# Performance work log

Measured on AMD Instinct MI355X. Metric: run time of the kernel, lower is better.

The kernel has to match this reference:

```python
import jax, jax.numpy as jnp
import numpy as np

B, C, H, W = 16, 128, 32, 32
CHOICES, OUT_C, OH, OW = 4, 128, 32, 32
INIT_WEIGHTS = [0.25, 0.25, 0.25, 0.25]
INIT_STD = 0.01


def setup_inputs() -> dict:
    key = jax.random.key(0)
    ks = jax.random.split(key, 6)
    x = jax.random.normal(ks[0], (B, C, H, W), dtype=jnp.float32)
    # 1x1 conv1d weights == dense matrices [out, in]; xavier-normal-ish scale
    Wq = jax.random.normal(ks[1], (C, C), dtype=jnp.float32) * (1.0 / np.sqrt(C))
    Wk = jax.random.normal(ks[2], (C, C), dtype=jnp.float32) * (1.0 / np.sqrt(C))
    Wv = jax.random.normal(ks[3], (CHOICES * OUT_C, C), dtype=jnp.float32) * (1.0 / np.sqrt(C))
    gamma = jnp.ones((1,), dtype=jnp.float32)  # learnable scalar (0 at init; use 1 to exercise math)
    # mask init: per-choice mean = init_weights[i] * out_choices, std = init_std
    means = jnp.asarray([w * CHOICES for w in INIT_WEIGHTS], dtype=jnp.float32)
    mask = jax.random.normal(ks[4], (1, OUT_C, OH, OW, CHOICES), dtype=jnp.float32) * INIT_STD + means
    return {"x": x, "Wq": Wq, "Wk": Wk, "Wv": Wv, "gamma": gamma, "mask": mask}


def reference(x, Wq, Wk, Wv, gamma, mask):
    b, c, h, w = x.shape
    n = h * w
    x2 = x.reshape(b, c, n)                                   # [b, C, N]
    f = jnp.einsum('oc,bcn->bon', Wq, x2)                     # query  [b, C, N]
    g = jnp.einsum('oc,bcn->bon', Wk, x2)                     # key    [b, C, N]
    hv = jnp.einsum('oc,bcn->bon', Wv, x2)                    # value  [b, CHOICES*OUT_C, N]
    # beta = softmax(f^T g) over dim 1 (rows), per torch code
    scores = jnp.einsum('bcn,bcm->bnm', f, g)                 # [b, N, N]
    beta = jax.nn.softmax(scores, axis=1)
    out = gamma * jnp.einsum('bkn,bnm->bkm', hv, beta)        # [b, CHOICES*OUT_C, N]
    out = out.reshape(b, CHOICES, OUT_C, OH, OW)              # no resize: H==OH, W==OW
    out = jnp.transpose(out, (0, 2, 3, 4, 1))                 # [b, OUT_C, OH, OW, CHOICES]
    return out + mask
```

## Files before the change

### kernel.cpp

```cpp
#include <hip/hip_runtime.h>

#define B 16
#define C 128
#define NN 1024
#define KV 512
#define CHO 4

typedef _Float16 f16x8 __attribute__((ext_vector_type(8)));
typedef float f32x4 __attribute__((ext_vector_type(4)));

__device__ __forceinline__ unsigned short f2h(float v) {
  _Float16 h = (_Float16)v;
  return __builtin_bit_cast(unsigned short, h);
}
__device__ __forceinline__ unsigned int packh2(float a, float b) {
  return (unsigned int)f2h(a) | ((unsigned int)f2h(b) << 16);
}

__global__ __launch_bounds__(256) void proj_kernel(
    const float* __restrict__ x, const float* __restrict__ Wq,
    const float* __restrict__ Wk, const float* __restrict__ Wv,
    unsigned short* __restrict__ fT, unsigned short* __restrict__ gT,
    unsigned short* __restrict__ hv)
{
  const int nt = blockIdx.x, rt = blockIdx.y, b = blockIdx.z;
  const int r0 = rt * 64, n0 = nt * 64;
  __shared__ __align__(16) float Wt[64][132];
  __shared__ __align__(16) float Xt[128][68];
  const int t = threadIdx.x;

  const float* Wbase; int roff;
  if (r0 < 128)      { Wbase = Wq; roff = r0; }
  else if (r0 < 256) { Wbase = Wk; roff = r0 - 128; }
  else               { Wbase = Wv; roff = r0 - 256; }

  #pragma unroll
  for (int i = 0; i < 8; ++i) {
    int idx = t + i * 256;
    int row = idx >> 5, c4 = (idx & 31) * 4;
    float4 v = *reinterpret_cast<const float4*>(Wbase + (size_t)(roff + row) * C + c4);
    *reinterpret_cast<float4*>(&Wt[row][c4]) = v;
  }
  #pragma unroll
  for (int i = 0; i < 8; ++i) {
    int idx = t + i * 256;
    int row = idx >> 4, c4 = (idx & 15) * 4;
    float4 v = *reinterpret_cast<const float4*>(x + (size_t)(b * C + row) * NN + n0 + c4);
    *reinterpret_cast<float4*>(&Xt[row][c4]) = v;
  }
  __syncthreads();

  const int tr = t >> 4, tc = t & 15;
  float acc[4][4];
  #pragma unroll
  for (int i = 0; i < 4; ++i)
    #pragma unroll
    for (int j = 0; j < 4; ++j) acc[i][j] = 0.f;

  for (int k = 0; k < C; k += 4) {
    float4 wv[4], xv[4];
    #pragma unroll
    for (int i = 0; i < 4; ++i) wv[i] = *reinterpret_cast<const float4*>(&Wt[tr * 4 + i][k]);
    #pragma unroll
    for (int kk = 0; kk < 4; ++kk) xv[kk] = *reinterpret_cast<const float4*>(&Xt[k + kk][tc * 4]);
    #pragma unroll
    for (int i = 0; i < 4; ++i) {
      float wi[4] = { wv[i].x, wv[i].y, wv[i].z, wv[i].w };
      #pragma unroll
      for (int kk = 0; kk < 4; ++kk) {
        float xk[4] = { xv[kk].x, xv[kk].y, xv[kk].z, xv[kk].w };
        acc[i][0] += wi[kk] * xk[0];
        acc[i][1] += wi[kk] * xk[1];
        acc[i][2] += wi[kk] * xk[2];
        acc[i][3] += wi[kk] * xk[3];
      }
    }
  }

  if (r0 < 256) {
    unsigned short* dst = (r0 < 128) ? fT : gT;
    #pragma unroll
    for (int j = 0; j < 4; ++j) {
      ushort4 o = { f2h(acc[0][j]), f2h(acc[1][j]), f2h(acc[2][j]), f2h(acc[3][j]) };
      *reinterpret_cast<ushort4*>(dst + ((size_t)(b * NN) + n0 + tc * 4 + j) * C + roff + tr * 4) = o;
    }
  } else {
    #pragma unroll
    for (int i = 0; i < 4; ++i) {
      ushort4 o = { f2h(acc[i][0]), f2h(acc[i][1]), f2h(acc[i][2]), f2h(acc[i][3]) };
      *reinterpret_cast<ushort4*>(hv + ((size_t)(b * KV) + roff + tr * 4 + i) * NN + n0 + tc * 4) = o;
    }
  }
}

__global__ __launch_bounds__(256, 2) void attn_kernel(
    const unsigned short* __restrict__ fT, const unsigned short* __restrict__ gT,
    const unsigned short* __restrict__ hv, const float* __restrict__ gamma,
    const float* __restrict__ mask, float* __restrict__ out)
{
  const int t  = threadIdx.x;
  const int w  = t >> 6;
  const int l  = t & 63;
  const int lg = l >> 4;
  const int lm = l & 15;
  const int b  = blockIdx.y;
  const int m0 = blockIdx.x * 64;

  __shared__ unsigned short P_lds[64][40];
  __shared__ float resc_s[64];
  __shared__ float lsum_s[64];

  f16x8 qf[4];
  {
    const unsigned short* qp = gT + ((size_t)(b * NN) + m0 + 16 * w + lm) * C + lg * 8;
    #pragma unroll
    for (int c4 = 0; c4 < 4; ++c4)
      qf[c4] = *reinterpret_cast<const f16x8*>(qp + c4 * 32);
  }

  f32x4 acc[8][4];
  #pragma unroll
  for (int kt = 0; kt < 8; ++kt)
    #pragma unroll
    for (int mt = 0; mt < 4; ++mt)
      acc[kt][mt] = (f32x4){0.f, 0.f, 0.f, 0.f};

  float M = -3.0e38f, Lpart = 0.f;

  const unsigned short* kp = fT + ((size_t)(b * NN) + lm) * C + lg * 8;
  const unsigned short* vp = hv + ((size_t)(b * KV) + 128 * w + lm) * NN + lg * 8;

  #pragma unroll 1
  for (int n0 = 0; n0 < NN; n0 += 32) {
    f16x8 vf[8];
    #pragma unroll
    for (int kt = 0; kt < 8; ++kt)
      vf[kt] = *reinterpret_cast<const f16x8*>(vp + (size_t)(16 * kt) * NN + n0);

    f32x4 st0 = {0.f, 0.f, 0.f, 0.f}, st1 = {0.f, 0.f, 0.f, 0.f};
    #pragma unroll
    for (int c4 = 0; c4 < 4; ++c4) {
      f16x8 k0 = *reinterpret_cast<const f16x8*>(kp + (size_t)(n0)      * C + c4 * 32);
      f16x8 k1 = *reinterpret_cast<const f16x8*>(kp + (size_t)(n0 + 16) * C + c4 * 32);
      st0 = __builtin_amdgcn_mfma_f32_16x16x32_f16(k0, qf[c4], st0, 0, 0, 0);
      st1 = __builtin_amdgcn_mfma_f32_16x16x32_f16(k1, qf[c4], st1, 0, 0, 0);
    }

    float cmax = fmaxf(fmaxf(fmaxf(st0.x, st0.y), fmaxf(st0.z, st0.w)),
                       fmaxf(fmaxf(st1.x, st1.y), fmaxf(st1.z, st1.w)));
    cmax = fmaxf(cmax, __shfl_xor(cmax, 16, 64));
    cmax = fmaxf(cmax, __shfl_xor(cmax, 32, 64));
    float r = 1.0f;
    if (!__all(cmax <= M + 8.0f)) {
      float newM = fmaxf(M, cmax);
      r = __expf(M - newM);
      M = newM;
      Lpart *= r;
    }
    float p0 = __expf(st0.x - M), p1 = __expf(st0.y - M),
          p2 = __expf(st0.z - M), p3 = __expf(st0.w - M),
          p4 = __expf(st1.x - M), p5 = __expf(st1.y - M),
          p6 = __expf(st1.z - M), p7 = __expf(st1.w - M);
    Lpart += ((p0 + p1) + (p2 + p3)) + ((p4 + p5) + (p6 + p7));
    if (lg == 0) resc_s[16 * w + lm] = r;
    unsigned short* prow = &P_lds[16 * w + lm][0];
    *(unsigned int*)(prow + 4 * lg)          = packh2(p0, p1);
    *(unsigned int*)(prow + 4 * lg + 2)      = packh2(p2, p3);
    *(unsigned int*)(prow + 16 + 4 * lg)     = packh2(p4, p5);
    *(unsigned int*)(prow + 16 + 4 * lg + 2) = packh2(p6, p7);
    __syncthreads();

    float rr0 = resc_s[lm], rr1 = resc_s[16 + lm], rr2 = resc_s[32 + lm], rr3 = resc_s[48 + lm];
    if (!__all((rr0 == 1.f) & (rr1 == 1.f) & (rr2 == 1.f) & (rr3 == 1.f))) {
      float rr[4] = { rr0, rr1, rr2, rr3 };
      #pragma unroll
      for (int kt = 0; kt < 8; ++kt)
        #pragma unroll
        for (int mt = 0; mt < 4; ++mt)
          acc[kt][mt] *= rr[mt];
    }

    f16x8 pt[4];
    #pragma unroll
    for (int mt = 0; mt < 4; ++mt)
      pt[mt] = *reinterpret_cast<const f16x8*>(&P_lds[16 * mt + lm][8 * lg]);

    #pragma unroll
    for (int kt = 0; kt < 8; ++kt) {
      acc[kt][0] = __builtin_amdgcn_mfma_f32_16x16x32_f16(vf[kt], pt[0], acc[kt][0], 0, 0, 0);
      acc[kt][1] = __builtin_amdgcn_mfma_f32_16x16x32_f16(vf[kt], pt[1], acc[kt][1], 0, 0, 0);
      acc[kt][2] = __builtin_amdgcn_mfma_f32_16x16x32_f16(vf[kt], pt[2], acc[kt][2], 0, 0, 0);
      acc[kt][3] = __builtin_amdgcn_mfma_f32_16x16x32_f16(vf[kt], pt[3], acc[kt][3], 0, 0, 0);
    }
    __syncthreads();
  }

  float Lp = Lpart;
  Lp += __shfl_xor(Lp, 16, 64);
  Lp += __shfl_xor(Lp, 32, 64);
  if (lg == 0) lsum_s[16 * w + lm] = Lp;
  __syncthreads();

  const float gam = gamma[0];
  float scv[4] = { gam / lsum_s[lm],      gam / lsum_s[16 + lm],
                   gam / lsum_s[32 + lm], gam / lsum_s[48 + lm] };

  #pragma unroll
  for (int kt = 0; kt < 8; ++kt) {
    #pragma unroll
    for (int mt = 0; mt < 4; ++mt) {
      #pragma unroll
      for (int reg = 0; reg < 4; ++reg) {
        int oc = 16 * kt + 4 * lg + reg;
        int m  = m0 + 16 * mt + lm;
        float v = acc[kt][mt][reg] * scv[mt] + mask[((size_t)oc * NN + m) * CHO + w];
        out[(((size_t)(b * 128 + oc)) * NN + m) * CHO + w] = v;
      }
    }
  }
}

extern "C" void kernel_launch(void* const* d_in, const int* in_sizes, int n_in,
                              void* d_out, int out_size, void* d_ws, size_t ws_size,
                              hipStream_t stream) {
  const float* x     = (const float*)d_in[0];
  const float* Wq    = (const float*)d_in[1];
  const float* Wk    = (const float*)d_in[2];
  const float* Wv    = (const float*)d_in[3];
  const float* gamma = (const float*)d_in[4];
  const float* mask  = (const float*)d_in[5];
  float* out = (float*)d_out;

  unsigned short* fT = (unsigned short*)d_ws;
  unsigned short* gT = fT + (size_t)B * NN * C;
  unsigned short* hv = gT + (size_t)B * NN * C;

  proj_kernel<<<dim3(16, 12, B), 256, 0, stream>>>(x, Wq, Wk, Wv, fT, gT, hv);
  attn_kernel<<<dim3(16, B), 256, 0, stream>>>(fT, gT, hv, gamma, mask, out);
}
```

Measured before the change: 128.7 us.

## Use MFMA for projections and split attention into more, smaller blocks

The projection kernel now converts x to fp16 in shared memory and uses 16x16x32 MFMA instructions instead of scalar fp32 FMAs. Its grid is flattened and swizzled across XCDs. The attention kernel now uses 32-query blocks with 8 waves: 2 waves compute scores and all 8 split the 512 value rows. This gives 512 blocks instead of 256 and halves the accumulator registers. The cost is recomputing scores redundantly across waves (4x per query tile), extra K loads, and fp16 rounding of x and the weights before projection.

```diff
diff --git a/kernel.cpp b/kernel.cpp
--- a/kernel.cpp
+++ b/kernel.cpp
@@ -16,125 +16,133 @@
 __device__ __forceinline__ unsigned int packh2(float a, float b) {
   return (unsigned int)f2h(a) | ((unsigned int)f2h(b) << 16);
 }
-
-__global__ __launch_bounds__(256) void proj_kernel(
+__device__ __forceinline__ f16x8 ldcvt8(const float* __restrict__ p) {
+  float4 a = *reinterpret_cast<const float4*>(p);
+  float4 b = *reinterpret_cast<const float4*>(p + 4);
+  f16x8 r;
+  r[0] = (_Float16)a.x; r[1] = (_Float16)a.y; r[2] = (_Float16)a.z; r[3] = (_Float16)a.w;
+  r[4] = (_Float16)b.x; r[5] = (_Float16)b.y; r[6] = (_Float16)b.z; r[7] = (_Float16)b.w;
+  return r;
+}
+
+__global__ __launch_bounds__(256, 4) void proj_kernel(
     const float* __restrict__ x, const float* __restrict__ Wq,
     const float* __restrict__ Wk, const float* __restrict__ Wv,
     unsigned short* __restrict__ fT, unsigned short* __restrict__ gT,
     unsigned short* __restrict__ hv)
 {
-  const int nt = blockIdx.x, rt = blockIdx.y, b = blockIdx.z;
-  const int r0 = rt * 64, n0 = nt * 64;
-  __shared__ __align__(16) float Wt[64][132];
-  __shared__ __align__(16) float Xt[128][68];
+  int wg = blockIdx.x;
+  wg = (wg & 7) * 384 + (wg >> 3);
+  const int b   = wg / 192;
+  const int rem = wg % 192;
+  const int rt  = rem % 12;
+  const int n0  = (rem / 12) * 64;
+
+  __shared__ __align__(16) unsigned short XT[64][136];
+
   const int t = threadIdx.x;
-
-  const float* Wbase; int roff;
-  if (r0 < 128)      { Wbase = Wq; roff = r0; }
-  else if (r0 < 256) { Wbase = Wk; roff = r0 - 128; }
-  else               { Wbase = Wv; roff = r0 - 256; }
-
-  #pragma unroll
-  for (int i = 0; i < 8; ++i) {
-    int idx = t + i * 256;
-    int row = idx >> 5, c4 = (idx & 31) * 4;
-    float4 v = *reinterpret_cast<const float4*>(Wbase + (size_t)(roff + row) * C + c4);
-    *reinterpret_cast<float4*>(&Wt[row][c4]) = v;
-  }
-  #pragma unroll
-  for (int i = 0; i < 8; ++i) {
-    int idx = t + i * 256;
-    int row = idx >> 4, c4 = (idx & 15) * 4;
-    float4 v = *reinterpret_cast<const float4*>(x + (size_t)(b * C + row) * NN + n0 + c4);
-    *reinterpret_cast<float4*>(&Xt[row][c4]) = v;
+  const int w = t >> 6, l = t & 63, lg = l >> 4, lm = l & 15;
+
+  {
+    const float* xb = x + (size_t)b * C * NN;
+    #pragma unroll
+    for (int i = 0; i < 8; ++i) {
+      int flat = t + i * 256;
+      int c  = flat >> 4;
+      int ng = flat & 15;
+      float4 v = *reinterpret_cast<const float4*>(xb + (size_t)c * NN + n0 + ng * 4);
+      XT[ng * 4 + 0][c] = f2h(v.x);
+      XT[ng * 4 + 1][c] = f2h(v.y);
+      XT[ng * 4 + 2][c] = f2h(v.z);
+      XT[ng * 4 + 3][c] = f2h(v.w);
+    }
   }
   __syncthreads();
 
-  const int tr = t >> 4, tc = t & 15;
-  float acc[4][4];
-  #pragma unroll
-  for (int i = 0; i < 4; ++i)
-    #pragma unroll
-    for (int j = 0; j < 4; ++j) acc[i][j] = 0.f;
-
-  for (int k = 0; k < C; k += 4) {
-    float4 wv[4], xv[4];
-    #pragma unroll
-    for (int i = 0; i < 4; ++i) wv[i] = *reinterpret_cast<const float4*>(&Wt[tr * 4 + i][k]);
-    #pragma unroll
-    for (int kk = 0; kk < 4; ++kk) xv[kk] = *reinterpret_cast<const float4*>(&Xt[k + kk][tc * 4]);
-    #pragma unroll
-    for (int i = 0; i < 4; ++i) {
-      float wi[4] = { wv[i].x, wv[i].y, wv[i].z, wv[i].w };
-      #pragma unroll
-      for (int kk = 0; kk < 4; ++kk) {
-        float xk[4] = { xv[kk].x, xv[kk].y, xv[kk].z, xv[kk].w };
-        acc[i][0] += wi[kk] * xk[0];
-        acc[i][1] += wi[kk] * xk[1];
-        acc[i][2] += wi[kk] * xk[2];
-        acc[i][3] += wi[kk] * xk[3];
-      }
-    }
-  }
-
-  if (r0 < 256) {
-    unsigned short* dst = (r0 < 128) ? fT : gT;
-    #pragma unroll
-    for (int j = 0; j < 4; ++j) {
-      ushort4 o = { f2h(acc[0][j]), f2h(acc[1][j]), f2h(acc[2][j]), f2h(acc[3][j]) };
-      *reinterpret_cast<ushort4*>(dst + ((size_t)(b * NN) + n0 + tc * 4 + j) * C + roff + tr * 4) = o;
+  if (rt < 4) {
+    const float* Wsrc = (rt < 2) ? Wq : Wk;
+    unsigned short* dst = (rt < 2) ? fT : gT;
+    const int c0 = (rt & 1) * 64;
+    const int r  = c0 + 16 * w + lm;
+    f16x8 af[4];
+    #pragma unroll
+    for (int c4 = 0; c4 < 4; ++c4)
+      af[c4] = ldcvt8(Wsrc + (size_t)r * C + c4 * 32 + lg * 8);
+    #pragma unroll
+    for (int nt4 = 0; nt4 < 4; ++nt4) {
+      f32x4 acc = {0.f, 0.f, 0.f, 0.f};
+      #pragma unroll
+      for (int c4 = 0; c4 < 4; ++c4) {
+        f16x8 xb = *reinterpret_cast<const f16x8*>(&XT[16 * nt4 + lm][c4 * 32 + lg * 8]);
+        acc = __builtin_amdgcn_mfma_f32_16x16x32_f16(af[c4], xb, acc, 0, 0, 0);
+      }
+      int n = n0 + 16 * nt4 + lm;
+      ushort4 o = { f2h(acc[0]), f2h(acc[1]), f2h(acc[2]), f2h(acc[3]) };
+      *reinterpret_cast<ushort4*>(dst + ((size_t)(b * NN) + n) * C + c0 + 16 * w + 4 * lg) = o;
     }
   } else {
-    #pragma unroll
-    for (int i = 0; i < 4; ++i) {
-      ushort4 o = { f2h(acc[i][0]), f2h(acc[i][1]), f2h(acc[i][2]), f2h(acc[i][3]) };
-      *reinterpret_cast<ushort4*>(hv + ((size_t)(b * KV) + roff + tr * 4 + i) * NN + n0 + tc * 4) = o;
-    }
-  }
-}
-
-__global__ __launch_bounds__(256, 2) void attn_kernel(
+    const int kk = (rt - 4) * 64 + 16 * w + lm;
+    f16x8 wb[4];
+    #pragma unroll
+    for (int c4 = 0; c4 < 4; ++c4)
+      wb[c4] = ldcvt8(Wv + (size_t)kk * C + c4 * 32 + lg * 8);
+    #pragma unroll
+    for (int nt4 = 0; nt4 < 4; ++nt4) {
+      f32x4 acc = {0.f, 0.f, 0.f, 0.f};
+      #pragma unroll
+      for (int c4 = 0; c4 < 4; ++c4) {
+        f16x8 xa = *reinterpret_cast<const f16x8*>(&XT[16 * nt4 + lm][c4 * 32 + lg * 8]);
+        acc = __builtin_amdgcn_mfma_f32_16x16x32_f16(xa, wb[c4], acc, 0, 0, 0);
+      }
+      ushort4 o = { f2h(acc[0]), f2h(acc[1]), f2h(acc[2]), f2h(acc[3]) };
+      *reinterpret_cast<ushort4*>(hv + ((size_t)(b * KV) + kk) * NN + n0 + 16 * nt4 + 4 * lg) = o;
+    }
+  }
+}
+
+__global__ __launch_bounds__(512, 4) void attn_kernel(
     const unsigned short* __restrict__ fT, const unsigned short* __restrict__ gT,
     const unsigned short* __restrict__ hv, const float* __restrict__ gamma,
     const float* __restrict__ mask, float* __restrict__ out)
 {
-  const int t  = threadIdx.x;
-  const int w  = t >> 6;
-  const int l  = t & 63;
-  const int lg = l >> 4;
-  const int lm = l & 15;
-  const int b  = blockIdx.y;
-  const int m0 = blockIdx.x * 64;
-
-  __shared__ unsigned short P_lds[64][40];
-  __shared__ float resc_s[64];
-  __shared__ float lsum_s[64];
+  int wg = blockIdx.x;
+  wg = (wg & 7) * 64 + (wg >> 3);
+  const int b  = wg >> 5;
+  const int m0 = (wg & 31) * 32;
+
+  const int t = threadIdx.x;
+  const int w = t >> 6, l = t & 63, lg = l >> 4, lm = l & 15;
+  const int ms = w & 1;
+
+  __shared__ __align__(16) unsigned short P_lds[32][40];
+  __shared__ float resc_s[32];
+  __shared__ float lsum_s[32];
 
   f16x8 qf[4];
   {
-    const unsigned short* qp = gT + ((size_t)(b * NN) + m0 + 16 * w + lm) * C + lg * 8;
+    const unsigned short* qp = gT + ((size_t)(b * NN) + m0 + 16 * ms + lm) * C + lg * 8;
     #pragma unroll
     for (int c4 = 0; c4 < 4; ++c4)
       qf[c4] = *reinterpret_cast<const f16x8*>(qp + c4 * 32);
   }
 
-  f32x4 acc[8][4];
+  f32x4 acc[4][2];
   #pragma unroll
-  for (int kt = 0; kt < 8; ++kt)
-    #pragma unroll
-    for (int mt = 0; mt < 4; ++mt)
-      acc[kt][mt] = (f32x4){0.f, 0.f, 0.f, 0.f};
+  for (int kt = 0; kt < 4; ++kt) {
+    acc[kt][0] = (f32x4){0.f, 0.f, 0.f, 0.f};
+    acc[kt][1] = (f32x4){0.f, 0.f, 0.f, 0.f};
+  }
 
   float M = -3.0e38f, Lpart = 0.f;
 
   const unsigned short* kp = fT + ((size_t)(b * NN) + lm) * C + lg * 8;
-  const unsigned short* vp = hv + ((size_t)(b * KV) + 128 * w + lm) * NN + lg * 8;
+  const unsigned short* vp = hv + ((size_t)(b * KV) + 64 * w + lm) * NN + lg * 8;
 
   #pragma unroll 1
   for (int n0 = 0; n0 < NN; n0 += 32) {
-    f16x8 vf[8];
-    #pragma unroll
-    for (int kt = 0; kt < 8; ++kt)
+    f16x8 vf[4];
+    #pragma unroll
+    for (int kt = 0; kt < 4; ++kt)
       vf[kt] = *reinterpret_cast<const f16x8*>(vp + (size_t)(16 * kt) * NN + n0);
 
     f32x4 st0 = {0.f, 0.f, 0.f, 0.f}, st1 = {0.f, 0.f, 0.f, 0.f};
@@ -162,35 +170,32 @@
           p4 = __expf(st1.x - M), p5 = __expf(st1.y - M),
           p6 = __expf(st1.z - M), p7 = __expf(st1.w - M);
     Lpart += ((p0 + p1) + (p2 + p3)) + ((p4 + p5) + (p6 + p7));
-    if (lg == 0) resc_s[16 * w + lm] = r;
-    unsigned short* prow = &P_lds[16 * w + lm][0];
-    *(unsigned int*)(prow + 4 * lg)          = packh2(p0, p1);
-    *(unsigned int*)(prow + 4 * lg + 2)      = packh2(p2, p3);
-    *(unsigned int*)(prow + 16 + 4 * lg)     = packh2(p4, p5);
-    *(unsigned int*)(prow + 16 + 4 * lg + 2) = packh2(p6, p7);
+    if (w < 2) {
+      if (lg == 0) resc_s[16 * w + lm] = r;
+      unsigned short* prow = &P_lds[16 * w + lm][0];
+      *(unsigned int*)(prow + 4 * lg)          = packh2(p0, p1);
+      *(unsigned int*)(prow + 4 * lg + 2)      = packh2(p2, p3);
+      *(unsigned int*)(prow + 16 + 4 * lg)     = packh2(p4, p5);
+      *(unsigned int*)(prow + 16 + 4 * lg + 2) = packh2(p6, p7);
+    }
     __syncthreads();
 
-    float rr0 = resc_s[lm], rr1 = resc_s[16 + lm], rr2 = resc_s[32 + lm], rr3 = resc_s[48 + lm];
-    if (!__all((rr0 == 1.f) & (rr1 == 1.f) & (rr2 == 1.f) & (rr3 == 1.f))) {
-      float rr[4] = { rr0, rr1, rr2, rr3 };
-      #pragma unroll
-      for (int kt = 0; kt < 8; ++kt)
-        #pragma unroll
-        for (int mt = 0; mt < 4; ++mt)
-          acc[kt][mt] *= rr[mt];
-    }
-
-    f16x8 pt[4];
-    #pragma unroll
-    for (int mt = 0; mt < 4; ++mt)
-      pt[mt] = *reinterpret_cast<const f16x8*>(&P_lds[16 * mt + lm][8 * lg]);
-
-    #pragma unroll
-    for (int kt = 0; kt < 8; ++kt) {
-      acc[kt][0] = __builtin_amdgcn_mfma_f32_16x16x32_f16(vf[kt], pt[0], acc[kt][0], 0, 0, 0);
-      acc[kt][1] = __builtin_amdgcn_mfma_f32_16x16x32_f16(vf[kt], pt[1], acc[kt][1], 0, 0, 0);
-      acc[kt][2] = __builtin_amdgcn_mfma_f32_16x16x32_f16(vf[kt], pt[2], acc[kt][2], 0, 0, 0);
-      acc[kt][3] = __builtin_amdgcn_mfma_f32_16x16x32_f16(vf[kt], pt[3], acc[kt][3], 0, 0, 0);
+    float rr0 = resc_s[lm], rr1 = resc_s[16 + lm];
+    if (!__all((rr0 == 1.f) & (rr1 == 1.f))) {
+      #pragma unroll
+      for (int kt = 0; kt < 4; ++kt) {
+        acc[kt][0] *= rr0;
+        acc[kt][1] *= rr1;
+      }
+    }
+
+    f16x8 pt0 = *reinterpret_cast<const f16x8*>(&P_lds[lm][8 * lg]);
+    f16x8 pt1 = *reinterpret_cast<const f16x8*>(&P_lds[16 + lm][8 * lg]);
+
+    #pragma unroll
+    for (int kt = 0; kt < 4; ++kt) {
+      acc[kt][0] = __builtin_amdgcn_mfma_f32_16x16x32_f16(vf[kt], pt0, acc[kt][0], 0, 0, 0);
+      acc[kt][1] = __builtin_amdgcn_mfma_f32_16x16x32_f16(vf[kt], pt1, acc[kt][1], 0, 0, 0);
     }
     __syncthreads();
   }
@@ -198,23 +203,25 @@
   float Lp = Lpart;
   Lp += __shfl_xor(Lp, 16, 64);
   Lp += __shfl_xor(Lp, 32, 64);
-  if (lg == 0) lsum_s[16 * w + lm] = Lp;
+  if (w < 2 && lg == 0) lsum_s[16 * w + lm] = Lp;
   __syncthreads();
 
   const float gam = gamma[0];
-  float scv[4] = { gam / lsum_s[lm],      gam / lsum_s[16 + lm],
-                   gam / lsum_s[32 + lm], gam / lsum_s[48 + lm] };
+  const float scv0 = gam / lsum_s[lm];
+  const float scv1 = gam / lsum_s[16 + lm];
 
   #pragma unroll
-  for (int kt = 0; kt < 8; ++kt) {
-    #pragma unroll
-    for (int mt = 0; mt < 4; ++mt) {
+  for (int kt = 0; kt < 4; ++kt) {
+    #pragma unroll
+    for (int mt = 0; mt < 2; ++mt) {
+      float sc = mt ? scv1 : scv0;
+      int m = m0 + 16 * mt + lm;
       #pragma unroll
       for (int reg = 0; reg < 4; ++reg) {
-        int oc = 16 * kt + 4 * lg + reg;
-        int m  = m0 + 16 * mt + lm;
-        float v = acc[kt][mt][reg] * scv[mt] + mask[((size_t)oc * NN + m) * CHO + w];
-        out[(((size_t)(b * 128 + oc)) * NN + m) * CHO + w] = v;
+        int k  = 64 * w + 16 * kt + 4 * lg + reg;
+        int oc = k & 127, ch = k >> 7;
+        float v = acc[kt][mt][reg] * sc + mask[((size_t)oc * NN + m) * CHO + ch];
+        out[(((size_t)(b * 128 + oc)) * NN + m) * CHO + ch] = v;
       }
     }
   }
@@ -235,6 +242,6 @@
   unsigned short* gT = fT + (size_t)B * NN * C;
   unsigned short* hv = gT + (size_t)B * NN * C;
 
-  proj_kernel<<<dim3(16, 12, B), 256, 0, stream>>>(x, Wq, Wk, Wv, fT, gT, hv);
-  attn_kernel<<<dim3(16, B), 256, 0, stream>>>(fT, gT, hv, gamma, mask, out);
-}
+  proj_kernel<<<dim3(3072), 256, 0, stream>>>(x, Wq, Wk, Wv, fT, gT, hv);
+  attn_kernel<<<dim3(512), 512, 0, stream>>>(fT, gT, hv, gamma, mask, out);
+}
```

Measured after the change: 213.1 us. +65.6%, slower.
